# Performance work log

Hardware: AMD Instinct MI355X
Metric: run time of the kernel (lower is better)

Reference implementation:

```python
import jax, jax.numpy as jnp
import numpy as np

B, Q, HID = 8, 8, 4096
H, KVH, D = 32, 8, 128
KV = 4096
ROPE_THETA = 10000.0


def rotate_half(x):
    x1, x2 = jnp.split(x, 2, axis=-1)
    return jnp.concatenate([-x2, x1], axis=-1)


def setup_inputs() -> dict:
    key = jax.random.key(0)
    ks = jax.random.split(key, 6)
    hidden_states = jax.random.normal(ks[0], (B, Q, HID), dtype=jnp.float32)
    position_ids = jnp.broadcast_to(jnp.arange(KV, dtype=jnp.int64), (B, KV))
    key_cache = jax.random.normal(ks[1], (B, KVH, KV, D), dtype=jnp.float32)
    value_cache = jax.random.normal(ks[2], (B, KVH, KV, D), dtype=jnp.float32)
    # mask: True -> blocked (-10000). Queries occupy last Q positions, causal.
    qpos = KV - Q + jnp.arange(Q)
    attention_mask = (jnp.arange(KV)[None, :] > qpos[:, None])[None, None]  # [1,1,Q,KV]
    attention_mask = jnp.broadcast_to(attention_mask, (B, 1, Q, KV))
    q_w = jax.random.normal(ks[3], (HID, HID), dtype=jnp.float32) * 0.02
    o_w = jax.random.normal(ks[4], (HID, HID), dtype=jnp.float32) * 0.02
    return {"hidden_states": hidden_states, "position_ids": position_ids,
            "key_cache": key_cache, "value_cache": value_cache,
            "attention_mask": attention_mask, "q_w": q_w, "o_w": o_w}


def reference(hidden_states, position_ids, key_cache, value_cache, attention_mask, q_w, o_w):
    # q projection: nn.Linear -> x @ W^T
    q = hidden_states @ q_w.T                       # [B,Q,HID]
    q = q.reshape(B, Q, H, D).transpose(0, 2, 1, 3)  # [B,H,Q,D]

    # rotary tables for kv_seq_len positions
    half = D // 2
    inv_freq = 1.0 / (ROPE_THETA ** (jnp.arange(0, half, dtype=jnp.float32) / half))
    t = jnp.arange(KV, dtype=jnp.float32)
    freqs = t[:, None] * inv_freq[None, :]           # [KV, D/2]
    emb = jnp.concatenate([freqs, freqs], axis=-1)   # [KV, D]
    cos_t, sin_t = jnp.cos(emb), jnp.sin(emb)

    # position_idx trick from the module: single effective rope position
    idx = jnp.argmax(position_ids.astype(jnp.int32), axis=1)[0]
    pid = jnp.take(position_ids, idx[None], axis=1)  # [B,1]
    cos = cos_t[pid][:, None]                        # [B,1,1,D]
    sin = sin_t[pid][:, None]
    q = q * cos + rotate_half(q) * sin               # [B,H,Q,D]

    # GQA attention without materializing repeat_kv (same math)
    G = H // KVH
    qg = q.reshape(B, KVH, G, Q, D)
    scores = jnp.einsum('bkgqd,bksd->bkgqs', qg, key_cache) / jnp.sqrt(jnp.float32(D))
    mask = attention_mask[:, :, None]                # [B,1,1,Q,KV]
    scores = jnp.where(mask, jnp.float32(-10000.0), scores)
    probs = jax.nn.softmax(scores.astype(jnp.float32), axis=-1).astype(q.dtype)
    out = jnp.einsum('bkgqs,bksd->bkgqd', probs, value_cache)  # [B,KVH,G,Q,D]
    out = out.reshape(B, H, Q, D).transpose(0, 2, 1, 3).reshape(B, Q, HID)
    return out @ o_w.T
```

## Files before the change

kernel.cpp:

```cpp
#include <hip/hip_runtime.h>
#include <math.h>

#define B_   8
#define Q_   8
#define HID  4096
#define NH   32
#define KVH_ 8
#define GQ   4
#define D_   128
#define KV_  4096
#define M_   64

#define KC_  8

#define OFF_COS   0
#define OFF_SIN   512
#define OFF_QROPE 1024
#define OFF_ATT   (OFF_QROPE + M_*HID)
#define OFF_OPART (OFF_ATT + M_*HID)
#define OFF_MPART (OFF_OPART + 64*8*32*128)
#define OFF_LPART (OFF_MPART + 64*8*32)
#define OFF_GPART (OFF_LPART + 64*8*32)

typedef __attribute__((ext_vector_type(8))) short short8;
typedef __attribute__((ext_vector_type(4))) float f32x4;

__global__ void prep_kernel(const int* __restrict__ pos, float* __restrict__ ws) {
    __shared__ int sv[256], si[256];
    __shared__ int s_idx;
    int t = threadIdx.x;
    int bv = -2147483647 - 1, bi = 0x7fffffff;
    for (int i = t; i < KV_; i += 256) {
        int v = pos[i];
        if (v > bv || (v == bv && i < bi)) { bv = v; bi = i; }
    }
    sv[t] = bv; si[t] = bi;
    __syncthreads();
    for (int off = 128; off > 0; off >>= 1) {
        if (t < off) {
            int v2 = sv[t + off], i2 = si[t + off];
            if (v2 > sv[t] || (v2 == sv[t] && i2 < si[t])) { sv[t] = v2; si[t] = i2; }
        }
        __syncthreads();
    }
    if (t == 0) s_idx = si[0];
    __syncthreads();
    int idx = s_idx;
    for (int u = t; u < B_ * 64; u += 256) {
        int b = u >> 6, d = u & 63;
        int pid = pos[b * KV_ + idx];
        float inv = __expf(-(float)d * (9.210340371976184f / 64.0f));
        float f = (float)pid * inv;
        ws[OFF_COS + u] = cosf(f);
        ws[OFF_SIN + u] = sinf(f);
    }
}

__device__ __forceinline__ unsigned f2bf_rne(float x) {
    unsigned u = __float_as_uint(x);
    return (u + 0x7fffu + ((u >> 16) & 1u)) >> 16;
}
__device__ __forceinline__ float bf2f(unsigned h) { return __uint_as_float(h << 16); }

__device__ __forceinline__ void cvt4(float4 v, uint2* h2, uint2* l2) {
    float f[4] = {v.x, v.y, v.z, v.w};
    unsigned h[4], l[4];
    #pragma unroll
    for (int i = 0; i < 4; ++i) {
        h[i] = f2bf_rne(f[i]);
        l[i] = f2bf_rne(f[i] - bf2f(h[i]));
    }
    h2->x = h[0] | (h[1] << 16); h2->y = h[2] | (h[3] << 16);
    l2->x = l[0] | (l[1] << 16); l2->y = l[2] | (l[3] << 16);
}

__global__ __launch_bounds__(256) void gemm_part(const float* __restrict__ A,
                                                 const float* __restrict__ W,
                                                 float* __restrict__ part) {
    __shared__ __align__(16) unsigned short AH[2][64][64];
    __shared__ __align__(16) unsigned short AL[2][64][64];
    __shared__ __align__(16) unsigned short WH[2][64][64];
    __shared__ __align__(16) unsigned short WL[2][64][64];

    int nc = blockIdx.x, kc = blockIdx.y;
    int t = threadIdx.x;
    int k0 = kc * 512, n0 = nc * 64;
    int f4 = t & 15;
    int rb = t >> 4;
    int oct = f4 >> 1;
    int sub = (f4 & 1) * 4;

    f32x4 acc[4];
    #pragma unroll
    for (int ct = 0; ct < 4; ++ct) acc[ct] = (f32x4){0.f, 0.f, 0.f, 0.f};

    {
        #pragma unroll
        for (int i = 0; i < 4; ++i) {
            int r = rb + 16 * i;
            float4 va = *(const float4*)(A + (size_t)r * HID + k0 + f4 * 4);
            float4 vw = *(const float4*)(W + (size_t)(n0 + r) * HID + k0 + f4 * 4);
            int slot = ((oct ^ (r & 7)) * 8 + sub);
            uint2 h2, l2;
            cvt4(va, &h2, &l2);
            *(uint2*)&AH[0][r][slot] = h2; *(uint2*)&AL[0][r][slot] = l2;
            cvt4(vw, &h2, &l2);
            *(uint2*)&WH[0][r][slot] = h2; *(uint2*)&WL[0][r][slot] = l2;
        }
    }
    __syncthreads();

    int w = t >> 6, l = t & 63;
    int rA = 16 * w + (l & 15);
    int sA = rA & 7;
    int lq = l >> 4;
    int cur = 0;

    for (int kt = 0; kt < 8; ++kt) {
        float4 va[4], vw[4];
        if (kt < 7) {
            #pragma unroll
            for (int i = 0; i < 4; ++i) {
                int r = rb + 16 * i;
                va[i] = *(const float4*)(A + (size_t)r * HID + k0 + (kt + 1) * 64 + f4 * 4);
                vw[i] = *(const float4*)(W + (size_t)(n0 + r) * HID + k0 + (kt + 1) * 64 + f4 * 4);
            }
        }
        #pragma unroll
        for (int ks = 0; ks < 2; ++ks) {
            int o2 = ks * 4 + lq;
            short8 ah = *(const short8*)&AH[cur][rA][(o2 ^ sA) * 8];
            short8 al = *(const short8*)&AL[cur][rA][(o2 ^ sA) * 8];
            #pragma unroll
            for (int ct = 0; ct < 4; ++ct) {
                int nB = ct * 16 + (l & 15);
                int sB = nB & 7;
                short8 bh = *(const short8*)&WH[cur][nB][(o2 ^ sB) * 8];
                short8 bl = *(const short8*)&WL[cur][nB][(o2 ^ sB) * 8];
                acc[ct] = __builtin_amdgcn_mfma_f32_16x16x32_bf16(ah, bh, acc[ct], 0, 0, 0);
                acc[ct] = __builtin_amdgcn_mfma_f32_16x16x32_bf16(ah, bl, acc[ct], 0, 0, 0);
                acc[ct] = __builtin_amdgcn_mfma_f32_16x16x32_bf16(al, bh, acc[ct], 0, 0, 0);
            }
        }
        if (kt < 7) {
            int nb = cur ^ 1;
            #pragma unroll
            for (int i = 0; i < 4; ++i) {
                int r = rb + 16 * i;
                int slot = ((oct ^ (r & 7)) * 8 + sub);
                uint2 h2, l2;
                cvt4(va[i], &h2, &l2);
                *(uint2*)&AH[nb][r][slot] = h2; *(uint2*)&AL[nb][r][slot] = l2;
                cvt4(vw[i], &h2, &l2);
                *(uint2*)&WH[nb][r][slot] = h2; *(uint2*)&WL[nb][r][slot] = l2;
            }
            __syncthreads();
            cur = nb;
        }
    }

    #pragma unroll
    for (int ct = 0; ct < 4; ++ct) {
        int n = n0 + ct * 16 + (l & 15);
        #pragma unroll
        for (int i = 0; i < 4; ++i) {
            int m = 16 * w + lq * 4 + i;
            part[((size_t)kc * 64 + m) * HID + n] = acc[ct][i];
        }
    }
}

__global__ void qrope_kernel(float* ws) {
    const float* part = ws + OFF_GPART;
    int blk = blockIdx.x;
    int b = blk >> 5, h = blk & 31;
    int t = threadIdx.x;
    int qq = t >> 5, dl = t & 31;
    int m = b * 8 + qq;
    int d0 = dl * 2;
    float x0 = 0, x1 = 0, y0 = 0, y1 = 0;
    const float* pbase = part + (size_t)m * HID + h * 128;
    #pragma unroll
    for (int kc = 0; kc < KC_; ++kc) {
        const float* p = pbase + (size_t)kc * 64 * HID;
        x0 += p[d0];      x1 += p[d0 + 1];
        y0 += p[d0 + 64]; y1 += p[d0 + 65];
    }
    float c0 = ws[OFF_COS + b * 64 + d0], c1 = ws[OFF_COS + b * 64 + d0 + 1];
    float s0 = ws[OFF_SIN + b * 64 + d0], s1 = ws[OFF_SIN + b * 64 + d0 + 1];
    float* qr = ws + OFF_QROPE + ((size_t)(b * 32 + h)) * Q_ * D_ + (size_t)qq * D_;
    qr[d0]      = x0 * c0 - y0 * s0;
    qr[d0 + 1]  = x1 * c1 - y1 * s1;
    qr[d0 + 64] = y0 * c0 + x0 * s0;
    qr[d0 + 65] = y1 * c1 + x1 * s1;
}

#define CHUNK 512
#define TK 64
__global__ __launch_bounds__(256) void attn_kernel(const float* __restrict__ Kc,
                                                   const float* __restrict__ Vc,
                                                   float* __restrict__ ws) {
    __shared__ __align__(16) float qT[128][36];
    __shared__ __align__(16) float kT[128][68];
    __shared__ __align__(16) float pT[64][36];
    __shared__ float m_st[32], l_st[32], al_st[32];

    int c = blockIdx.x, kvh = blockIdx.y, b = blockIdx.z;
    int t = threadIdx.x;
    int pair = b * 8 + kvh;
    const float* qbase = ws + OFF_QROPE + (size_t)pair * 32 * 128;
    {
        int r = t & 31, qh = t >> 5;
        #pragma unroll
        for (int cq = 0; cq < 4; ++cq) {
            int dq = qh + cq * 8;
            float4 v = *(const float4*)(qbase + (size_t)r * 128 + dq * 4);
            qT[dq*4+0][r] = v.x; qT[dq*4+1][r] = v.y;
            qT[dq*4+2][r] = v.z; qT[dq*4+3][r] = v.w;
        }
    }
    if (t < 32) { m_st[t] = -INFINITY; l_st[t] = 0.f; }

    int st = t & 15;
    int dh = (t >> 4) & 1;
    int rt = t >> 5;
    int dt = t & 31;

    float o[4][4];
    #pragma unroll
    for (int i = 0; i < 4; i++)
        #pragma unroll
        for (int j = 0; j < 4; j++) o[i][j] = 0.f;

    const float* Kb = Kc + ((size_t)pair * KV_ + c * CHUNK) * D_;
    const float* Vb = Vc + ((size_t)pair * KV_ + c * CHUNK) * D_;
    const float scale = 0.08838834764831845f;

    int sk = t >> 2, qr = t & 3;
    float4 kreg[8];
    {
        const float* kr = Kb + (size_t)sk * D_ + qr * 4;
        #pragma unroll
        for (int cq = 0; cq < 8; ++cq) kreg[cq] = *(const float4*)(kr + cq * 16);
    }

    for (int T = 0; T < CHUNK / TK; ++T) {
        int s0 = T * TK;
        __syncthreads();
        {
            #pragma unroll
            for (int cq = 0; cq < 8; ++cq) {
                int d = qr * 4 + cq * 16;
                kT[d+0][sk] = kreg[cq].x; kT[d+1][sk] = kreg[cq].y;
                kT[d+2][sk] = kreg[cq].z; kT[d+3][sk] = kreg[cq].w;
            }
        }
        if (T < CHUNK / TK - 1) {
            const float* kr = Kb + (size_t)((T + 1) * TK + sk) * D_ + qr * 4;
            #pragma unroll
            for (int cq = 0; cq < 8; ++cq) kreg[cq] = *(const float4*)(kr + cq * 16);
        }
        __syncthreads();
        float S[4][4];
        #pragma unroll
        for (int i = 0; i < 4; i++)
            #pragma unroll
            for (int j = 0; j < 4; j++) S[i][j] = 0.f;
        int dbase = dh * 64;
        #pragma unroll 4
        for (int dd = 0; dd < 64; ++dd) {
            int d = dbase + dd;
            float4 q4 = *(const float4*)&qT[d][rt * 4];
            float4 k4 = *(const float4*)&kT[d][st * 4];
            float qa[4] = {q4.x, q4.y, q4.z, q4.w};
            float ka[4] = {k4.x, k4.y, k4.z, k4.w};
            #pragma unroll
            for (int i = 0; i < 4; i++)
            #pragma unroll
            for (int j = 0; j < 4; j++)
                S[i][j] += qa[i] * ka[j];
        }
        #pragma unroll
        for (int i = 0; i < 4; i++)
            #pragma unroll
            for (int j = 0; j < 4; j++)
                S[i][j] += __shfl_xor(S[i][j], 16, 64);
        int sabs_base = c * CHUNK + s0 + st * 4;
        #pragma unroll
        for (int i = 0; i < 4; i++) {
            int r = rt * 4 + i;
            int qq = r & 7;
            int qpos = KV_ - Q_ + qq;
            float v[4];
            float rmax = -INFINITY;
            #pragma unroll
            for (int j = 0; j < 4; j++) {
                int sa = sabs_base + j;
                float x = (sa > qpos) ? -10000.0f : S[i][j] * scale;
                v[j] = x;
                rmax = fmaxf(rmax, x);
            }
            for (int ml = 1; ml <= 8; ml <<= 1) rmax = fmaxf(rmax, __shfl_xor(rmax, ml, 64));
            float m_old = m_st[r];
            float m_new = fmaxf(m_old, rmax);
            float al = __expf(m_old - m_new);
            float ps = 0.f;
            #pragma unroll
            for (int j = 0; j < 4; j++) {
                float p = __expf(v[j] - m_new);
                if (dh == 0) pT[st * 4 + j][r] = p;
                ps += p;
            }
            for (int ml = 1; ml <= 8; ml <<= 1) ps += __shfl_xor(ps, ml, 64);
            if (st == 0 && dh == 0) {
                l_st[r] = l_st[r] * al + ps;
                m_st[r] = m_new;
                al_st[r] = al;
            }
        }
        __syncthreads();
        float al4[4];
        #pragma unroll
        for (int i = 0; i < 4; i++) al4[i] = al_st[rt * 4 + i];
        #pragma unroll
        for (int i = 0; i < 4; i++)
            #pragma unroll
            for (int j = 0; j < 4; j++) o[i][j] *= al4[i];
        const float* Vg = Vb + (size_t)s0 * D_ + dt * 4;
        #pragma unroll 8
        for (int s = 0; s < TK; ++s) {
            float4 p4 = *(const float4*)&pT[s][rt * 4];
            float4 v4 = *(const float4*)(Vg + (size_t)s * D_);
            float pp[4] = {p4.x, p4.y, p4.z, p4.w};
            float vv[4] = {v4.x, v4.y, v4.z, v4.w};
            #pragma unroll
            for (int i = 0; i < 4; i++)
            #pragma unroll
            for (int j = 0; j < 4; j++)
                o[i][j] += pp[i] * vv[j];
        }
    }
    float* opart = ws + OFF_OPART + ((size_t)pair * 8 + c) * 32 * 128;
    #pragma unroll
    for (int i = 0; i < 4; i++) {
        int r = rt * 4 + i;
        float* dst = opart + (size_t)r * 128 + dt * 4;
        float4 v;
        v.x = o[i][0]; v.y = o[i][1]; v.z = o[i][2]; v.w = o[i][3];
        *(float4*)dst = v;
    }
    __syncthreads();
    if (t < 32) {
        ws[OFF_MPART + ((size_t)pair * 8 + c) * 32 + t] = m_st[t];
        ws[OFF_LPART + ((size_t)pair * 8 + c) * 32 + t] = l_st[t];
    }
}

__global__ void combine_kernel(float* ws) {
    __shared__ float w_sh[8][32];
    int pair = blockIdx.x;
    int b = pair >> 3, kvh = pair & 7;
    int t = threadIdx.x;
    if (t < 32) {
        int r = t;
        float M = -INFINITY;
        float mv[8];
        #pragma unroll
        for (int cc = 0; cc < 8; ++cc) {
            mv[cc] = ws[OFF_MPART + ((size_t)pair * 8 + cc) * 32 + r];
            M = fmaxf(M, mv[cc]);
        }
        float L = 0.f;
        float e[8];
        #pragma unroll
        for (int cc = 0; cc < 8; ++cc) {
            e[cc] = __expf(mv[cc] - M);
            L += e[cc] * ws[OFF_LPART + ((size_t)pair * 8 + cc) * 32 + r];
        }
        float invL = 1.f / L;
        #pragma unroll
        for (int cc = 0; cc < 8; ++cc) w_sh[cc][r] = e[cc] * invL;
    }
    __syncthreads();
    const float* opart = ws + OFF_OPART + (size_t)pair * 8 * 32 * 128;
    float* aout = ws + OFF_ATT;
    for (int idx = t; idx < 32 * 128; idx += 256) {
        int r = idx >> 7, d = idx & 127;
        float acc = 0.f;
        #pragma unroll
        for (int cc = 0; cc < 8; ++cc)
            acc += w_sh[cc][r] * opart[((size_t)cc * 32 + r) * 128 + d];
        int g = r >> 3, qq = r & 7;
        aout[((size_t)(b * 8 + qq)) * HID + (kvh * 4 + g) * 128 + d] = acc;
    }
}

__global__ void oreduce_kernel(const float* __restrict__ part, float* __restrict__ out) {
    int idx = blockIdx.x * 256 + threadIdx.x;
    float4 acc = {0, 0, 0, 0};
    const float4* p = (const float4*)part;
    #pragma unroll
    for (int kc = 0; kc < KC_; ++kc) {
        float4 v = p[(size_t)kc * 65536 + idx];
        acc.x += v.x; acc.y += v.y; acc.z += v.z; acc.w += v.w;
    }
    ((float4*)out)[idx] = acc;
}

extern "C" void kernel_launch(void* const* d_in, const int* in_sizes, int n_in,
                              void* d_out, int out_size, void* d_ws, size_t ws_size,
                              hipStream_t stream) {
    const float* hidden = (const float*)d_in[0];
    const int*   pos    = (const int*)d_in[1];
    const float* kcache = (const float*)d_in[2];
    const float* vcache = (const float*)d_in[3];
    const float* qw = (const float*)d_in[5];
    const float* ow = (const float*)d_in[6];
    float* ws  = (float*)d_ws;
    float* out = (float*)d_out;
    float* gpart = ws + OFF_GPART;

    prep_kernel<<<1, 256, 0, stream>>>(pos, ws);
    gemm_part<<<dim3(64, KC_), 256, 0, stream>>>(hidden, qw, gpart);
    qrope_kernel<<<256, 256, 0, stream>>>(ws);
    attn_kernel<<<dim3(8, 8, 8), 256, 0, stream>>>(kcache, vcache, ws);
    combine_kernel<<<64, 256, 0, stream>>>(ws);
    gemm_part<<<dim3(64, KC_), 256, 0, stream>>>(ws + OFF_ATT, ow, gpart);
    oreduce_kernel<<<256, 256, 0, stream>>>(gpart, out);
}
```

Baseline: 432.8 us.

## Compute attention QK^T scores with split-bf16 MFMA instead of scalar FMA

The QK^T score computation in the attention kernel moves from a scalar fp32 outer-product loop to bf16 MFMA instructions. Q and K are split into high and low bf16 parts and three MFMAs recover near-fp32 accuracy. K and Q are now stored in swizzled bf16 shared-memory layouts, and the softmax max and sum reductions are restructured into cross-wave shared-memory reductions, which adds an extra barrier per tile. The PV product stays scalar, and the conversion work adds ALU cost.

Measured after the change: 417.1 us. 1.04x faster.

```diff
diff --git a/kernel.cpp b/kernel.cpp
--- a/kernel.cpp
+++ b/kernel.cpp
@@ -72,6 +72,20 @@
     }
     h2->x = h[0] | (h[1] << 16); h2->y = h[2] | (h[3] << 16);
     l2->x = l[0] | (l[1] << 16); l2->y = l[2] | (l[3] << 16);
+}
+
+__device__ __forceinline__ void cvt_oct(float4 a, float4 b, uint4* h4, uint4* l4v) {
+    float f[8] = {a.x, a.y, a.z, a.w, b.x, b.y, b.z, b.w};
+    unsigned h[8], lo[8];
+    #pragma unroll
+    for (int i = 0; i < 8; ++i) {
+        h[i] = f2bf_rne(f[i]);
+        lo[i] = f2bf_rne(f[i] - bf2f(h[i]));
+    }
+    h4->x  = h[0]  | (h[1]  << 16); h4->y  = h[2]  | (h[3]  << 16);
+    h4->z  = h[4]  | (h[5]  << 16); h4->w  = h[6]  | (h[7]  << 16);
+    l4v->x = lo[0] | (lo[1] << 16); l4v->y = lo[2] | (lo[3] << 16);
+    l4v->z = lo[4] | (lo[5] << 16); l4v->w = lo[6] | (lo[7] << 16);
 }
 
 __global__ __launch_bounds__(256) void gemm_part(const float* __restrict__ A,
@@ -200,133 +214,162 @@
 __global__ __launch_bounds__(256) void attn_kernel(const float* __restrict__ Kc,
                                                    const float* __restrict__ Vc,
                                                    float* __restrict__ ws) {
-    __shared__ __align__(16) float qT[128][36];
-    __shared__ __align__(16) float kT[128][68];
+    __shared__ __align__(16) unsigned short KSh[64][128];
+    __shared__ __align__(16) unsigned short KSl[64][128];
+    __shared__ __align__(16) unsigned short QSh[32][128];
+    __shared__ __align__(16) unsigned short QSl[32][128];
     __shared__ __align__(16) float pT[64][36];
+    __shared__ float wm[4][32], wsum[4][32];
     __shared__ float m_st[32], l_st[32], al_st[32];
 
     int c = blockIdx.x, kvh = blockIdx.y, b = blockIdx.z;
     int t = threadIdx.x;
     int pair = b * 8 + kvh;
     const float* qbase = ws + OFF_QROPE + (size_t)pair * 32 * 128;
+
     {
-        int r = t & 31, qh = t >> 5;
-        #pragma unroll
-        for (int cq = 0; cq < 4; ++cq) {
-            int dq = qh + cq * 8;
-            float4 v = *(const float4*)(qbase + (size_t)r * 128 + dq * 4);
-            qT[dq*4+0][r] = v.x; qT[dq*4+1][r] = v.y;
-            qT[dq*4+2][r] = v.z; qT[dq*4+3][r] = v.w;
-        }
+        int qrow = t >> 3, seg = t & 7;
+        const float* qs = qbase + (size_t)qrow * 128 + seg * 16;
+        float4 a0 = *(const float4*)(qs + 0);
+        float4 a1 = *(const float4*)(qs + 4);
+        float4 a2 = *(const float4*)(qs + 8);
+        float4 a3 = *(const float4*)(qs + 12);
+        uint4 h4, l4v;
+        cvt_oct(a0, a1, &h4, &l4v);
+        int s0_ = ((seg * 2 + 0) ^ (qrow & 7)) * 8;
+        *(uint4*)&QSh[qrow][s0_] = h4; *(uint4*)&QSl[qrow][s0_] = l4v;
+        cvt_oct(a2, a3, &h4, &l4v);
+        int s1_ = ((seg * 2 + 1) ^ (qrow & 7)) * 8;
+        *(uint4*)&QSh[qrow][s1_] = h4; *(uint4*)&QSl[qrow][s1_] = l4v;
     }
     if (t < 32) { m_st[t] = -INFINITY; l_st[t] = 0.f; }
 
-    int st = t & 15;
-    int dh = (t >> 4) & 1;
-    int rt = t >> 5;
-    int dt = t & 31;
-
-    float o[4][4];
-    #pragma unroll
-    for (int i = 0; i < 4; i++)
-        #pragma unroll
-        for (int j = 0; j < 4; j++) o[i][j] = 0.f;
-
+    int w = t >> 6, l = t & 63;
+    int l15 = l & 15, l4g = l >> 4;
+    int key = l15 & 7;
+    int sArow = 16 * w + l15;
+
+    int sq = t >> 4, od = t & 15;
     const float* Kb = Kc + ((size_t)pair * KV_ + c * CHUNK) * D_;
     const float* Vb = Vc + ((size_t)pair * KV_ + c * CHUNK) * D_;
     const float scale = 0.08838834764831845f;
 
-    int sk = t >> 2, qr = t & 3;
     float4 kreg[8];
     {
-        const float* kr = Kb + (size_t)sk * D_ + qr * 4;
-        #pragma unroll
-        for (int cq = 0; cq < 8; ++cq) kreg[cq] = *(const float4*)(kr + cq * 16);
-    }
+        const float* kr = Kb + (size_t)(4 * sq) * D_ + od * 8;
+        #pragma unroll
+        for (int i = 0; i < 4; ++i) {
+            kreg[2 * i]     = *(const float4*)(kr + (size_t)i * D_);
+            kreg[2 * i + 1] = *(const float4*)(kr + (size_t)i * D_ + 4);
+        }
+    }
+
+    int rt = t >> 5, dt = t & 31;
+    float o[4][4];
+    #pragma unroll
+    for (int i = 0; i < 4; i++)
+        #pragma unroll
+        for (int j = 0; j < 4; j++) o[i][j] = 0.f;
 
     for (int T = 0; T < CHUNK / TK; ++T) {
-        int s0 = T * TK;
+        {
+            #pragma unroll
+            for (int i = 0; i < 4; ++i) {
+                int s = 4 * sq + i;
+                uint4 h4, l4v;
+                cvt_oct(kreg[2 * i], kreg[2 * i + 1], &h4, &l4v);
+                int slot = (od ^ (s & 7)) * 8;
+                *(uint4*)&KSh[s][slot] = h4;
+                *(uint4*)&KSl[s][slot] = l4v;
+            }
+        }
+        if (T < CHUNK / TK - 1) {
+            const float* kr = Kb + (size_t)((T + 1) * TK + 4 * sq) * D_ + od * 8;
+            #pragma unroll
+            for (int i = 0; i < 4; ++i) {
+                kreg[2 * i]     = *(const float4*)(kr + (size_t)i * D_);
+                kreg[2 * i + 1] = *(const float4*)(kr + (size_t)i * D_ + 4);
+            }
+        }
         __syncthreads();
-        {
-            #pragma unroll
-            for (int cq = 0; cq < 8; ++cq) {
-                int d = qr * 4 + cq * 16;
-                kT[d+0][sk] = kreg[cq].x; kT[d+1][sk] = kreg[cq].y;
-                kT[d+2][sk] = kreg[cq].z; kT[d+3][sk] = kreg[cq].w;
-            }
-        }
-        if (T < CHUNK / TK - 1) {
-            const float* kr = Kb + (size_t)((T + 1) * TK + sk) * D_ + qr * 4;
-            #pragma unroll
-            for (int cq = 0; cq < 8; ++cq) kreg[cq] = *(const float4*)(kr + cq * 16);
-        }
+
+        f32x4 S0 = (f32x4){0.f, 0.f, 0.f, 0.f};
+        f32x4 S1 = (f32x4){0.f, 0.f, 0.f, 0.f};
+        #pragma unroll
+        for (int ks = 0; ks < 4; ++ks) {
+            int so = 4 * ks + l4g;
+            int sl = (so ^ key) * 8;
+            short8 ah  = *(const short8*)&KSh[sArow][sl];
+            short8 alo = *(const short8*)&KSl[sArow][sl];
+            short8 bh0 = *(const short8*)&QSh[l15][sl];
+            short8 bl0 = *(const short8*)&QSl[l15][sl];
+            short8 bh1 = *(const short8*)&QSh[16 + l15][sl];
+            short8 bl1 = *(const short8*)&QSl[16 + l15][sl];
+            S0 = __builtin_amdgcn_mfma_f32_16x16x32_bf16(ah, bh0, S0, 0, 0, 0);
+            S0 = __builtin_amdgcn_mfma_f32_16x16x32_bf16(ah, bl0, S0, 0, 0, 0);
+            S0 = __builtin_amdgcn_mfma_f32_16x16x32_bf16(alo, bh0, S0, 0, 0, 0);
+            S1 = __builtin_amdgcn_mfma_f32_16x16x32_bf16(ah, bh1, S1, 0, 0, 0);
+            S1 = __builtin_amdgcn_mfma_f32_16x16x32_bf16(ah, bl1, S1, 0, 0, 0);
+            S1 = __builtin_amdgcn_mfma_f32_16x16x32_bf16(alo, bh1, S1, 0, 0, 0);
+        }
+
+        int sbase = c * CHUNK + T * TK + 16 * w + l4g * 4;
+        int qpos = KV_ - Q_ + key;
+        float v0[4], v1[4];
+        float rm0 = -INFINITY, rm1 = -INFINITY;
+        #pragma unroll
+        for (int j = 0; j < 4; ++j) {
+            int sa = sbase + j;
+            float x0 = (sa > qpos) ? -10000.0f : S0[j] * scale;
+            float x1 = (sa > qpos) ? -10000.0f : S1[j] * scale;
+            v0[j] = x0; v1[j] = x1;
+            rm0 = fmaxf(rm0, x0); rm1 = fmaxf(rm1, x1);
+        }
+        rm0 = fmaxf(rm0, __shfl_xor(rm0, 16, 64));
+        rm0 = fmaxf(rm0, __shfl_xor(rm0, 32, 64));
+        rm1 = fmaxf(rm1, __shfl_xor(rm1, 16, 64));
+        rm1 = fmaxf(rm1, __shfl_xor(rm1, 32, 64));
+        if (l < 16) { wm[w][l] = rm0; wm[w][16 + l] = rm1; }
         __syncthreads();
-        float S[4][4];
+
+        int q0 = l15, q1 = 16 + l15;
+        float tm0 = fmaxf(fmaxf(wm[0][q0], wm[1][q0]), fmaxf(wm[2][q0], wm[3][q0]));
+        float tm1 = fmaxf(fmaxf(wm[0][q1], wm[1][q1]), fmaxf(wm[2][q1], wm[3][q1]));
+        float mo0 = m_st[q0], mo1 = m_st[q1];
+        float mn0 = fmaxf(mo0, tm0), mn1 = fmaxf(mo1, tm1);
+        float al0 = __expf(mo0 - mn0), al1 = __expf(mo1 - mn1);
+        float ps0 = 0.f, ps1 = 0.f;
+        int srow = 16 * w + l4g * 4;
+        #pragma unroll
+        for (int j = 0; j < 4; ++j) {
+            float p0 = __expf(v0[j] - mn0);
+            float p1 = __expf(v1[j] - mn1);
+            pT[srow + j][q0] = p0;
+            pT[srow + j][q1] = p1;
+            ps0 += p0; ps1 += p1;
+        }
+        ps0 += __shfl_xor(ps0, 16, 64); ps0 += __shfl_xor(ps0, 32, 64);
+        ps1 += __shfl_xor(ps1, 16, 64); ps1 += __shfl_xor(ps1, 32, 64);
+        if (l < 16) { wsum[w][l] = ps0; wsum[w][16 + l] = ps1; }
+        if (w == 0 && l < 16) { al_st[l] = al0; al_st[16 + l] = al1; }
+        __syncthreads();
+
+        if (w == 0 && l < 32) {
+            float ts = wsum[0][l] + wsum[1][l] + wsum[2][l] + wsum[3][l];
+            float mn  = (l < 16) ? mn0 : mn1;
+            float alq = (l < 16) ? al0 : al1;
+            l_st[l] = l_st[l] * alq + ts;
+            m_st[l] = mn;
+        }
+
+        float al4[4];
+        #pragma unroll
+        for (int i = 0; i < 4; i++) al4[i] = al_st[rt * 4 + i];
         #pragma unroll
         for (int i = 0; i < 4; i++)
             #pragma unroll
-            for (int j = 0; j < 4; j++) S[i][j] = 0.f;
-        int dbase = dh * 64;
-        #pragma unroll 4
-        for (int dd = 0; dd < 64; ++dd) {
-            int d = dbase + dd;
-            float4 q4 = *(const float4*)&qT[d][rt * 4];
-            float4 k4 = *(const float4*)&kT[d][st * 4];
-            float qa[4] = {q4.x, q4.y, q4.z, q4.w};
-            float ka[4] = {k4.x, k4.y, k4.z, k4.w};
-            #pragma unroll
-            for (int i = 0; i < 4; i++)
-            #pragma unroll
-            for (int j = 0; j < 4; j++)
-                S[i][j] += qa[i] * ka[j];
-        }
-        #pragma unroll
-        for (int i = 0; i < 4; i++)
-            #pragma unroll
-            for (int j = 0; j < 4; j++)
-                S[i][j] += __shfl_xor(S[i][j], 16, 64);
-        int sabs_base = c * CHUNK + s0 + st * 4;
-        #pragma unroll
-        for (int i = 0; i < 4; i++) {
-            int r = rt * 4 + i;
-            int qq = r & 7;
-            int qpos = KV_ - Q_ + qq;
-            float v[4];
-            float rmax = -INFINITY;
-            #pragma unroll
-            for (int j = 0; j < 4; j++) {
-                int sa = sabs_base + j;
-                float x = (sa > qpos) ? -10000.0f : S[i][j] * scale;
-                v[j] = x;
-                rmax = fmaxf(rmax, x);
-            }
-            for (int ml = 1; ml <= 8; ml <<= 1) rmax = fmaxf(rmax, __shfl_xor(rmax, ml, 64));
-            float m_old = m_st[r];
-            float m_new = fmaxf(m_old, rmax);
-            float al = __expf(m_old - m_new);
-            float ps = 0.f;
-            #pragma unroll
-            for (int j = 0; j < 4; j++) {
-                float p = __expf(v[j] - m_new);
-                if (dh == 0) pT[st * 4 + j][r] = p;
-                ps += p;
-            }
-            for (int ml = 1; ml <= 8; ml <<= 1) ps += __shfl_xor(ps, ml, 64);
-            if (st == 0 && dh == 0) {
-                l_st[r] = l_st[r] * al + ps;
-                m_st[r] = m_new;
-                al_st[r] = al;
-            }
-        }
-        __syncthreads();
-        float al4[4];
-        #pragma unroll
-        for (int i = 0; i < 4; i++) al4[i] = al_st[rt * 4 + i];
-        #pragma unroll
-        for (int i = 0; i < 4; i++)
-            #pragma unroll
             for (int j = 0; j < 4; j++) o[i][j] *= al4[i];
-        const float* Vg = Vb + (size_t)s0 * D_ + dt * 4;
+        const float* Vg = Vb + (size_t)(T * TK) * D_ + dt * 4;
         #pragma unroll 8
         for (int s = 0; s < TK; ++s) {
             float4 p4 = *(const float4*)&pT[s][rt * 4];
```
